# Optimization experiments

Hardware: AMD Instinct MI355X
Metric: run time of the kernel (lower is better)

The kernel has to match this reference:

```python
import jax, jax.numpy as jnp
import numpy as np

B, H, W, C = 8, 64, 64, 256  # NHWC, SAGAN-style feature map


def setup_inputs() -> dict:
    key = jax.random.key(0)
    ks = jax.random.split(key, 10)
    d_qk, d_v = C // 8, C // 2
    sc = lambda fan_in: 1.0 / np.sqrt(fan_in)
    return {
        "x": jax.random.normal(ks[0], (B, H, W, C), dtype=jnp.float32),
        "Wf": jax.random.normal(ks[1], (C, d_qk), dtype=jnp.float32) * sc(C),
        "bf": jnp.zeros((d_qk,), dtype=jnp.float32),
        "Wg": jax.random.normal(ks[2], (C, d_qk), dtype=jnp.float32) * sc(C),
        "bg": jnp.zeros((d_qk,), dtype=jnp.float32),
        "Wh": jax.random.normal(ks[3], (C, d_v), dtype=jnp.float32) * sc(C),
        "bh": jnp.zeros((d_v,), dtype=jnp.float32),
        "Wo": jax.random.normal(ks[4], (d_v, C), dtype=jnp.float32) * sc(d_v),
        "bo": jnp.zeros((C,), dtype=jnp.float32),
        # original inits gamma=0.0 (identity fwd); use nonzero so fwd exercises attention
        "gamma": jnp.float32(0.5),
    }


def reference(x, Wf, bf, Wg, bg, Wh, bh, Wo, bo, gamma):
    b, h_, w_, c = x.shape
    n = h_ * w_
    xf = x.reshape(b, n, c)  # 1x1 convs are per-pixel GEMMs
    f = xf @ Wf + bf          # [B, N, C/8]  (keys)
    g = xf @ Wg + bg          # [B, N, C/8]  (queries)
    hv = xf @ Wh + bh         # [B, N, C/2]  (values)
    s = jnp.einsum('bnd,bmd->bnm', g, f)   # unscaled scores [B, N, N]
    beta = jax.nn.softmax(s, axis=-1)
    o = jnp.einsum('bnm,bmd->bnd', beta, hv)  # [B, N, C/2]
    o = o @ Wo + bo                           # output 1x1 conv -> [B, N, C]
    out = gamma * o + xf
    return out.reshape(b, h_, w_, c)
```

## Files before the change

kernel.cpp:

```cpp
#include <hip/hip_runtime.h>
#include <hip/hip_bf16.h>

#define NB   8
#define CC   256
#define NN   4096
#define NTOT (NB*NN)
#define DQK  32
#define DV   128

typedef __attribute__((ext_vector_type(8))) short bf16x8;
typedef __attribute__((ext_vector_type(4))) float f32x4;
typedef __attribute__((ext_vector_type(16))) float f32x16;
typedef __attribute__((ext_vector_type(4))) float float4v;
typedef __attribute__((ext_vector_type(4))) unsigned int u32x4;

__device__ __forceinline__ short f2bf(float f) {
    __hip_bfloat16 h = __float2bfloat16(f);
    return *reinterpret_cast<short*>(&h);
}
__device__ __forceinline__ float bf2f(short s) {
    unsigned int u = ((unsigned int)(unsigned short)s) << 16;
    return __builtin_bit_cast(float, u);
}
__device__ __forceinline__ unsigned int cvtpk(float lo, float hi) {
    unsigned int r;
    asm("v_cvt_pk_bf16_f32 %0, %1, %2" : "=v"(r) : "v"(lo), "v"(hi));
    return r;
}
__device__ __forceinline__ void plswap(unsigned int &a, unsigned int &b) {
    asm("v_permlane32_swap_b32 %0, %1" : "+v"(a), "+v"(b));
}

#define OFF_F     0u
#define OFF_G     (2u<<20)
#define OFF_VT    (4u<<20)
#define OFF_OP    (12u<<20)
#define OFF_LS    (28u<<20)
#define OFF_WQKVT ((28u<<20)+(512u<<10))
#define OFF_WOT   (OFF_WQKVT + 192u*256u*2u)

__global__ __launch_bounds__(256) void prep_kernel(
    const float* __restrict__ Wf, const float* __restrict__ Wg,
    const float* __restrict__ Wh, const float* __restrict__ Wo,
    short* __restrict__ WqkvT, short* __restrict__ WoT)
{
    int idx = blockIdx.x * 256 + threadIdx.x;
    if (idx < 192 * 256) {
        int j = idx >> 8, k = idx & 255;
        float v = (j < 32) ? Wf[k * 32 + j]
                : (j < 64) ? Wg[k * 32 + (j - 32)]
                           : Wh[k * 128 + (j - 64)];
        WqkvT[j * 256 + k] = f2bf(v);
    }
    int i2 = idx - 192 * 256;
    if (i2 >= 0 && i2 < 256 * 128) {
        int c = i2 >> 7, d = i2 & 127;
        WoT[c * 128 + d] = f2bf(Wo[d * 256 + c]);
    }
}

__global__ __launch_bounds__(256) void proj_kernel(
    const float* __restrict__ x,
    const float* __restrict__ bf_, const float* __restrict__ bg_,
    const float* __restrict__ bh_,
    const short* __restrict__ WqkvT,
    short* __restrict__ fws, short* __restrict__ gws, short* __restrict__ vtile)
{
    int wid = threadIdx.x >> 6, lane = threadIdx.x & 63;
    int col16 = lane & 15, rq = lane >> 4;
    int rbase = blockIdx.x * 64 + wid * 16;
    int arow = rbase + col16;

    f32x4 acc[12];
    #pragma unroll
    for (int i = 0; i < 12; ++i) acc[i] = (f32x4){0.f, 0.f, 0.f, 0.f};

    const float* xrow = x + (size_t)arow * CC;
    #pragma unroll
    for (int kk = 0; kk < 8; ++kk) {
        int k0 = kk * 32 + rq * 8;
        float4v u0 = *(const float4v*)(xrow + k0);
        float4v u1 = *(const float4v*)(xrow + k0 + 4);
        bf16x8 av;
        av[0]=f2bf(u0[0]); av[1]=f2bf(u0[1]); av[2]=f2bf(u0[2]); av[3]=f2bf(u0[3]);
        av[4]=f2bf(u1[0]); av[5]=f2bf(u1[1]); av[6]=f2bf(u1[2]); av[7]=f2bf(u1[3]);
        #pragma unroll
        for (int nf = 0; nf < 12; ++nf) {
            bf16x8 bv = *(const bf16x8*)(WqkvT + (nf * 16 + col16) * 256 + k0);
            acc[nf] = __builtin_amdgcn_mfma_f32_16x16x32_bf16(av, bv, acc[nf], 0, 0, 0);
        }
    }

    #pragma unroll
    for (int nf = 0; nf < 12; ++nf) {
        int colg = nf * 16 + col16;
        #pragma unroll
        for (int r = 0; r < 4; ++r) {
            int rowg = rbase + rq * 4 + r;
            float val = acc[nf][r];
            if (colg < 32) {
                fws[(size_t)rowg * DQK + colg] = f2bf(val + bf_[colg]);
            } else if (colg < 64) {
                int c = colg - 32;
                gws[(size_t)rowg * DQK + c] = f2bf((val + bg_[c]) * 1.44269504089f);
            } else {
                int d = colg - 64;
                int b = rowg >> 12, n = rowg & 4095;
                int kt = n >> 6, kslot = (n >> 4) & 3, klh = (n >> 3) & 1, j = n & 7;
                size_t addr = (((size_t)(b * 64 + kt) * 4 + kslot) * 2048)
                            + (d >> 5) * 512 + klh * 256 + (d & 31) * 8 + j;
                vtile[addr] = f2bf(val + bh_[d]);
            }
        }
    }
}

__global__ __launch_bounds__(256, 4) void attn_kernel(
    const short* __restrict__ fws, const short* __restrict__ gws,
    const short* __restrict__ vtile, short* __restrict__ opart,
    float* __restrict__ lspart)
{
    __shared__ __align__(16) char smem[33280];

    int t = threadIdx.x;
    int wid = t >> 6, lane = t & 63;
    int l31 = lane & 31, lh = lane >> 5;
    int qh = wid >> 1, kh = wid & 1;

    int bid = blockIdx.x;
    int sid = (bid & 7) * 128 + (bid >> 3);
    int b = sid >> 7, rem = sid & 127;
    int ksh = rem >> 6, qt = rem & 63;
    int qbase = b * NN + qt * 64;
    int k0 = ksh * 32, kend = k0 + 32;

    const short* grow = gws + (size_t)(qbase + qh * 32 + l31) * DQK;
    bf16x8 gb0 = *(const bf16x8*)(grow + lh * 8);
    bf16x8 gb1 = *(const bf16x8*)(grow + 16 + lh * 8);

    int foff = (kh * 32 + l31) * DQK + lh * 8;
    const short* fS = fws + (size_t)b * NN * DQK;
    bf16x8 fc0 = *(const bf16x8*)(fS + (size_t)k0 * 2048 + foff);
    bf16x8 fc1 = *(const bf16x8*)(fS + (size_t)k0 * 2048 + foff + 16);

    f32x16 oaccT[4], zero16;
    #pragma unroll
    for (int i = 0; i < 16; ++i) {
        zero16[i] = 0.f;
        oaccT[0][i] = 0.f; oaccT[1][i] = 0.f; oaccT[2][i] = 0.f; oaccT[3][i] = 0.f;
    }
    float lsum = 0.f;

    for (int kb = k0; kb < kend; ++kb) {
        const short* fnp = fS + (size_t)(kb + 1) * 2048 + foff;
        bf16x8 fn0 = *(const bf16x8*)(fnp);
        bf16x8 fn1 = *(const bf16x8*)(fnp + 16);

        f32x16 s = __builtin_amdgcn_mfma_f32_32x32x16_bf16(fc0, gb0, zero16, 0, 0, 0);
        s = __builtin_amdgcn_mfma_f32_32x32x16_bf16(fc1, gb1, s, 0, 0, 0);

        unsigned int w[8];
        #pragma unroll
        for (int i = 0; i < 8; ++i) {
            float pa = __builtin_exp2f(s[2 * i]);
            float pb = __builtin_exp2f(s[2 * i + 1]);
            lsum += pa + pb;
            w[i] = cvtpk(pa, pb);
        }
        plswap(w[0], w[2]); plswap(w[1], w[3]);
        plswap(w[4], w[6]); plswap(w[5], w[7]);

        const short* vb_kb = vtile + (((size_t)(b * 64 + kb) * 4 + kh * 2) * 2048)
                           + (size_t)lane * 8;
        #pragma unroll
        for (int ks = 0; ks < 2; ++ks) {
            u32x4 pw = { w[ks * 4], w[ks * 4 + 1], w[ks * 4 + 2], w[ks * 4 + 3] };
            bf16x8 pb_ = __builtin_bit_cast(bf16x8, pw);
            #pragma unroll
            for (int dt = 0; dt < 4; ++dt) {
                bf16x8 va = *(const bf16x8*)(vb_kb + ks * 2048 + dt * 512);
                oaccT[dt] = __builtin_amdgcn_mfma_f32_32x32x16_bf16(va, pb_, oaccT[dt], 0, 0, 0);
            }
        }
        fc0 = fn0; fc1 = fn1;
    }

    lsum += __shfl_xor(lsum, 32);
    float* lsbuf = (float*)(&smem[32768]);
    if (lh == 0) lsbuf[(qh * 2 + kh) * 32 + l31] = lsum;
    __syncthreads();

    char* obuf = smem;
    if (kh == 1) {
        #pragma unroll
        for (int dt = 0; dt < 4; ++dt) {
            #pragma unroll
            for (int r = 0; r < 16; ++r) {
                int d = dt * 32 + (r & 3) + 8 * (r >> 2) + 4 * lh;
                int q = qh * 32 + l31;
                int byte = q * 512 + ((((d >> 2) ^ (q & 31)) << 4) | ((d & 3) << 2));
                *(float*)(obuf + byte) = oaccT[dt][r];
            }
        }
    }
    __syncthreads();
    if (kh == 0) {
        float tot = lsbuf[qh * 64 + l31] + lsbuf[qh * 64 + 32 + l31];
        if (lh == 0) lspart[(size_t)(qbase + qh * 32 + l31) * 2 + ksh] = tot;
        float iv = 1.f / tot;
        #pragma unroll
        for (int dt = 0; dt < 4; ++dt) {
            #pragma unroll
            for (int r = 0; r < 16; ++r) {
                int d = dt * 32 + (r & 3) + 8 * (r >> 2) + 4 * lh;
                int q = qh * 32 + l31;
                int byte = q * 512 + ((((d >> 2) ^ (q & 31)) << 4) | ((d & 3) << 2));
                float* p = (float*)(obuf + byte);
                *p = (*p + oaccT[dt][r]) * iv;
            }
        }
    }
    __syncthreads();
    {
        int q = t >> 2, dg = t & 3;
        size_t orow = ((size_t)(qbase + q) * 2 + ksh) * 128 + dg * 32;
        #pragma unroll
        for (int cc = 0; cc < 8; cc += 2) {
            int c0 = dg * 8 + cc;
            f32x4 u0 = *(const f32x4*)(obuf + q * 512 + (((c0 ^ (q & 31)) << 4)));
            f32x4 u1 = *(const f32x4*)(obuf + q * 512 + ((((c0 + 1) ^ (q & 31)) << 4)));
            bf16x8 ov;
            ov[0]=f2bf(u0[0]); ov[1]=f2bf(u0[1]); ov[2]=f2bf(u0[2]); ov[3]=f2bf(u0[3]);
            ov[4]=f2bf(u1[0]); ov[5]=f2bf(u1[1]); ov[6]=f2bf(u1[2]); ov[7]=f2bf(u1[3]);
            *(bf16x8*)(opart + orow + cc * 4) = ov;
        }
    }
}

__global__ __launch_bounds__(256) void out_kernel(
    const short* __restrict__ opart, const float* __restrict__ lspart,
    const short* __restrict__ WoT,
    const float* __restrict__ bo, const float* __restrict__ gamma,
    const float* __restrict__ x, float* __restrict__ out)
{
    int wid = threadIdx.x >> 6, lane = threadIdx.x & 63;
    int col16 = lane & 15, rq = lane >> 4;
    int rbase = blockIdx.x * 64 + wid * 16;
    int arow = rbase + col16;

    float l0 = lspart[(size_t)arow * 2];
    float l1 = lspart[(size_t)arow * 2 + 1];
    float iv = 1.f / (l0 + l1);
    float w0 = l0 * iv, w1 = l1 * iv;

    const short* oprow = opart + (size_t)arow * 256;
    bf16x8 afr[4];
    #pragma unroll
    for (int kk = 0; kk < 4; ++kk) {
        bf16x8 a0 = *(const bf16x8*)(oprow + kk * 32 + rq * 8);
        bf16x8 a1 = *(const bf16x8*)(oprow + 128 + kk * 32 + rq * 8);
        bf16x8 af;
        #pragma unroll
        for (int j = 0; j < 8; ++j)
            af[j] = f2bf(w0 * bf2f(a0[j]) + w1 * bf2f(a1[j]));
        afr[kk] = af;
    }

    f32x4 acc[16];
    #pragma unroll
    for (int i = 0; i < 16; ++i) acc[i] = (f32x4){0.f, 0.f, 0.f, 0.f};

    #pragma unroll
    for (int nf = 0; nf < 16; ++nf) {
        #pragma unroll
        for (int kk = 0; kk < 4; ++kk) {
            bf16x8 bfr = *(const bf16x8*)(WoT + (nf * 16 + col16) * DV + kk * 32 + rq * 8);
            acc[nf] = __builtin_amdgcn_mfma_f32_16x16x32_bf16(afr[kk], bfr, acc[nf], 0, 0, 0);
        }
    }

    float gm = gamma[0];
    #pragma unroll
    for (int nf = 0; nf < 16; ++nf) {
        int colg = nf * 16 + col16;
        float bov = bo[colg];
        #pragma unroll
        for (int r = 0; r < 4; ++r) {
            int rowg = rbase + rq * 4 + r;
            out[(size_t)rowg * CC + colg] = gm * (acc[nf][r] + bov) + x[(size_t)rowg * CC + colg];
        }
    }
}

extern "C" void kernel_launch(void* const* d_in, const int* in_sizes, int n_in,
                              void* d_out, int out_size, void* d_ws, size_t ws_size,
                              hipStream_t stream)
{
    const float* x     = (const float*)d_in[0];
    const float* Wf    = (const float*)d_in[1];
    const float* bf_   = (const float*)d_in[2];
    const float* Wg    = (const float*)d_in[3];
    const float* bg_   = (const float*)d_in[4];
    const float* Wh    = (const float*)d_in[5];
    const float* bh_   = (const float*)d_in[6];
    const float* Wo    = (const float*)d_in[7];
    const float* bo    = (const float*)d_in[8];
    const float* gamma = (const float*)d_in[9];

    char* ws = (char*)d_ws;
    short* fws   = (short*)(ws + OFF_F);
    short* gws   = (short*)(ws + OFF_G);
    short* vtile = (short*)(ws + OFF_VT);
    short* opart = (short*)(ws + OFF_OP);
    float* lsp   = (float*)(ws + OFF_LS);
    short* WqkvT = (short*)(ws + OFF_WQKVT);
    short* WoT   = (short*)(ws + OFF_WOT);
    float* out   = (float*)d_out;

    hipLaunchKernelGGL(prep_kernel, dim3(320), dim3(256), 0, stream, Wf, Wg, Wh, Wo, WqkvT, WoT);
    hipLaunchKernelGGL(proj_kernel, dim3(512), dim3(256), 0, stream,
                       x, bf_, bg_, bh_, WqkvT, fws, gws, vtile);
    hipLaunchKernelGGL(attn_kernel, dim3(1024), dim3(256), 0, stream, fws, gws, vtile, opart, lsp);
    hipLaunchKernelGGL(out_kernel, dim3(512), dim3(256), 0, stream, opart, lsp, WoT, bo, gamma, x, out);
}
```

Baseline: 139.3 us.

## Double-buffer F and V register loads in attention loop with MFMA priority boost

The attention inner loop now prefetches both the key (F) fragments and all eight V fragments for the next key block into a second register set, alternating two buffers so global loads overlap the current block's MFMAs and exp work. Before, V was loaded just ahead of use. The PV MFMAs are wrapped in s_setprio to favour matrix issue, and launch bounds drop from 4 to 3 waves per SIMD to make room for the extra registers. The cost is lower occupancy and more VGPR pressure; loads at the loop tail are clamped to the last block, which adds a few redundant loads.

```diff
diff --git a/kernel.cpp b/kernel.cpp
--- a/kernel.cpp
+++ b/kernel.cpp
@@ -115,7 +115,7 @@
     }
 }
 
-__global__ __launch_bounds__(256, 4) void attn_kernel(
+__global__ __launch_bounds__(256, 3) void attn_kernel(
     const short* __restrict__ fws, const short* __restrict__ gws,
     const short* __restrict__ vtile, short* __restrict__ opart,
     float* __restrict__ lspart)
@@ -140,8 +140,8 @@
 
     int foff = (kh * 32 + l31) * DQK + lh * 8;
     const short* fS = fws + (size_t)b * NN * DQK;
-    bf16x8 fc0 = *(const bf16x8*)(fS + (size_t)k0 * 2048 + foff);
-    bf16x8 fc1 = *(const bf16x8*)(fS + (size_t)k0 * 2048 + foff + 16);
+    const short* vS = vtile + ((size_t)b * 64 * 4) * 2048 + (kh * 2) * 2048
+                    + (size_t)lane * 8;
 
     f32x16 oaccT[4], zero16;
     #pragma unroll
@@ -151,39 +151,63 @@
     }
     float lsum = 0.f;
 
-    for (int kb = k0; kb < kend; ++kb) {
-        const short* fnp = fS + (size_t)(kb + 1) * 2048 + foff;
-        bf16x8 fn0 = *(const bf16x8*)(fnp);
-        bf16x8 fn1 = *(const bf16x8*)(fnp + 16);
-
-        f32x16 s = __builtin_amdgcn_mfma_f32_32x32x16_bf16(fc0, gb0, zero16, 0, 0, 0);
-        s = __builtin_amdgcn_mfma_f32_32x32x16_bf16(fc1, gb1, s, 0, 0, 0);
-
-        unsigned int w[8];
-        #pragma unroll
-        for (int i = 0; i < 8; ++i) {
-            float pa = __builtin_exp2f(s[2 * i]);
-            float pb = __builtin_exp2f(s[2 * i + 1]);
-            lsum += pa + pb;
-            w[i] = cvtpk(pa, pb);
-        }
-        plswap(w[0], w[2]); plswap(w[1], w[3]);
-        plswap(w[4], w[6]); plswap(w[5], w[7]);
-
-        const short* vb_kb = vtile + (((size_t)(b * 64 + kb) * 4 + kh * 2) * 2048)
-                           + (size_t)lane * 8;
-        #pragma unroll
-        for (int ks = 0; ks < 2; ++ks) {
-            u32x4 pw = { w[ks * 4], w[ks * 4 + 1], w[ks * 4 + 2], w[ks * 4 + 3] };
-            bf16x8 pb_ = __builtin_bit_cast(bf16x8, pw);
-            #pragma unroll
-            for (int dt = 0; dt < 4; ++dt) {
-                bf16x8 va = *(const bf16x8*)(vb_kb + ks * 2048 + dt * 512);
-                oaccT[dt] = __builtin_amdgcn_mfma_f32_32x32x16_bf16(va, pb_, oaccT[dt], 0, 0, 0);
-            }
-        }
-        fc0 = fn0; fc1 = fn1;
-    }
+#define LOADSET(F0, F1, V0, V1, V2, V3, V4, V5, V6, V7, KB) {              \
+    int kc_ = (KB) < kend ? (KB) : kend - 1;                               \
+    const short* fp_ = fS + (size_t)kc_ * 2048 + foff;                     \
+    F0 = *(const bf16x8*)(fp_);                                            \
+    F1 = *(const bf16x8*)(fp_ + 16);                                       \
+    const short* vp_ = vS + (size_t)kc_ * 8192;                            \
+    V0 = *(const bf16x8*)(vp_);                                            \
+    V1 = *(const bf16x8*)(vp_ + 512);                                      \
+    V2 = *(const bf16x8*)(vp_ + 1024);                                     \
+    V3 = *(const bf16x8*)(vp_ + 1536);                                     \
+    V4 = *(const bf16x8*)(vp_ + 2048);                                     \
+    V5 = *(const bf16x8*)(vp_ + 2560);                                     \
+    V6 = *(const bf16x8*)(vp_ + 3072);                                     \
+    V7 = *(const bf16x8*)(vp_ + 3584);                                     \
+}
+
+#define COMPUTE(F0, F1, V0, V1, V2, V3, V4, V5, V6, V7) {                  \
+    f32x16 s_ = __builtin_amdgcn_mfma_f32_32x32x16_bf16(F0, gb0, zero16, 0, 0, 0); \
+    s_ = __builtin_amdgcn_mfma_f32_32x32x16_bf16(F1, gb1, s_, 0, 0, 0);    \
+    unsigned int w_[8];                                                    \
+    _Pragma("unroll")                                                      \
+    for (int i_ = 0; i_ < 8; ++i_) {                                       \
+        float pa_ = __builtin_exp2f(s_[2 * i_]);                           \
+        float pb_ = __builtin_exp2f(s_[2 * i_ + 1]);                       \
+        lsum += pa_ + pb_;                                                 \
+        w_[i_] = cvtpk(pa_, pb_);                                          \
+    }                                                                      \
+    plswap(w_[0], w_[2]); plswap(w_[1], w_[3]);                            \
+    plswap(w_[4], w_[6]); plswap(w_[5], w_[7]);                            \
+    u32x4 pw0_ = { w_[0], w_[1], w_[2], w_[3] };                           \
+    u32x4 pw1_ = { w_[4], w_[5], w_[6], w_[7] };                           \
+    bf16x8 p0_ = __builtin_bit_cast(bf16x8, pw0_);                         \
+    bf16x8 p1_ = __builtin_bit_cast(bf16x8, pw1_);                         \
+    __builtin_amdgcn_s_setprio(1);                                         \
+    oaccT[0] = __builtin_amdgcn_mfma_f32_32x32x16_bf16(V0, p0_, oaccT[0], 0, 0, 0); \
+    oaccT[1] = __builtin_amdgcn_mfma_f32_32x32x16_bf16(V1, p0_, oaccT[1], 0, 0, 0); \
+    oaccT[2] = __builtin_amdgcn_mfma_f32_32x32x16_bf16(V2, p0_, oaccT[2], 0, 0, 0); \
+    oaccT[3] = __builtin_amdgcn_mfma_f32_32x32x16_bf16(V3, p0_, oaccT[3], 0, 0, 0); \
+    oaccT[0] = __builtin_amdgcn_mfma_f32_32x32x16_bf16(V4, p1_, oaccT[0], 0, 0, 0); \
+    oaccT[1] = __builtin_amdgcn_mfma_f32_32x32x16_bf16(V5, p1_, oaccT[1], 0, 0, 0); \
+    oaccT[2] = __builtin_amdgcn_mfma_f32_32x32x16_bf16(V6, p1_, oaccT[2], 0, 0, 0); \
+    oaccT[3] = __builtin_amdgcn_mfma_f32_32x32x16_bf16(V7, p1_, oaccT[3], 0, 0, 0); \
+    __builtin_amdgcn_s_setprio(0);                                         \
+}
+
+    bf16x8 fa0, fa1, a0, a1, a2, a3, a4, a5, a6, a7;
+    bf16x8 fb0, fb1, b0, b1, b2, b3, b4, b5, b6, b7;
+
+    LOADSET(fa0, fa1, a0, a1, a2, a3, a4, a5, a6, a7, k0);
+    for (int kb = k0; kb < kend; kb += 2) {
+        LOADSET(fb0, fb1, b0, b1, b2, b3, b4, b5, b6, b7, kb + 1);
+        COMPUTE(fa0, fa1, a0, a1, a2, a3, a4, a5, a6, a7);
+        LOADSET(fa0, fa1, a0, a1, a2, a3, a4, a5, a6, a7, kb + 2);
+        COMPUTE(fb0, fb1, b0, b1, b2, b3, b4, b5, b6, b7);
+    }
+#undef LOADSET
+#undef COMPUTE
 
     lsum += __shfl_xor(lsum, 32);
     float* lsbuf = (float*)(&smem[32768]);
```

Result: slower. 256.5 us (+84.1%).

## Fuse output projection into attention kernel and split keys across waves

Applied to the files above, without the earlier changes.

Merges the attention and output-projection kernels. Each block now handles 32 queries over all 4096 keys, with the four waves striding over key tiles and reducing their partial accumulators through shared memory. The normalized result is written to LDS as bf16 and multiplied by Wo with MFMA, followed by the bias, gamma and residual epilogue. This removes the opart/lspart round trip through global memory and one launch, and adds setprio hints around the PV MFMAs. In exchange it adds an in-block cross-wave reduction, and each block now reads the whole key/value set for only 32 queries.

```diff
diff --git a/kernel.cpp b/kernel.cpp
--- a/kernel.cpp
+++ b/kernel.cpp
@@ -13,14 +13,11 @@
 typedef __attribute__((ext_vector_type(16))) float f32x16;
 typedef __attribute__((ext_vector_type(4))) float float4v;
 typedef __attribute__((ext_vector_type(4))) unsigned int u32x4;
+typedef __attribute__((ext_vector_type(2))) unsigned int u32x2;
 
 __device__ __forceinline__ short f2bf(float f) {
     __hip_bfloat16 h = __float2bfloat16(f);
     return *reinterpret_cast<short*>(&h);
-}
-__device__ __forceinline__ float bf2f(short s) {
-    unsigned int u = ((unsigned int)(unsigned short)s) << 16;
-    return __builtin_bit_cast(float, u);
 }
 __device__ __forceinline__ unsigned int cvtpk(float lo, float hi) {
     unsigned int r;
@@ -34,9 +31,7 @@
 #define OFF_F     0u
 #define OFF_G     (2u<<20)
 #define OFF_VT    (4u<<20)
-#define OFF_OP    (12u<<20)
-#define OFF_LS    (28u<<20)
-#define OFF_WQKVT ((28u<<20)+(512u<<10))
+#define OFF_WQKVT (12u<<20)
 #define OFF_WOT   (OFF_WQKVT + 192u*256u*2u)
 
 __global__ __launch_bounds__(256) void prep_kernel(
@@ -115,33 +110,29 @@
     }
 }
 
-__global__ __launch_bounds__(256, 4) void attn_kernel(
+__global__ __launch_bounds__(256, 4) void attn_fused_kernel(
     const short* __restrict__ fws, const short* __restrict__ gws,
-    const short* __restrict__ vtile, short* __restrict__ opart,
-    float* __restrict__ lspart)
+    const short* __restrict__ vtile, const short* __restrict__ WoT,
+    const float* __restrict__ bo, const float* __restrict__ gamma,
+    const float* __restrict__ x, float* __restrict__ out)
 {
     __shared__ __align__(16) char smem[33280];
 
     int t = threadIdx.x;
     int wid = t >> 6, lane = t & 63;
     int l31 = lane & 31, lh = lane >> 5;
-    int qh = wid >> 1, kh = wid & 1;
 
     int bid = blockIdx.x;
     int sid = (bid & 7) * 128 + (bid >> 3);
-    int b = sid >> 7, rem = sid & 127;
-    int ksh = rem >> 6, qt = rem & 63;
-    int qbase = b * NN + qt * 64;
-    int k0 = ksh * 32, kend = k0 + 32;
-
-    const short* grow = gws + (size_t)(qbase + qh * 32 + l31) * DQK;
+    int b = sid >> 7, qt = sid & 127;
+    int nbase = qt * 32;
+
+    const short* grow = gws + (size_t)(b * NN + nbase + l31) * DQK;
     bf16x8 gb0 = *(const bf16x8*)(grow + lh * 8);
     bf16x8 gb1 = *(const bf16x8*)(grow + 16 + lh * 8);
 
-    int foff = (kh * 32 + l31) * DQK + lh * 8;
-    const short* fS = fws + (size_t)b * NN * DQK;
-    bf16x8 fc0 = *(const bf16x8*)(fS + (size_t)k0 * 2048 + foff);
-    bf16x8 fc1 = *(const bf16x8*)(fS + (size_t)k0 * 2048 + foff + 16);
+    const short* fS = fws + (size_t)b * NN * DQK + l31 * DQK + lh * 8;
+    const short* vS = vtile + (size_t)b * 524288 + (size_t)lane * 8;
 
     f32x16 oaccT[4], zero16;
     #pragma unroll
@@ -151,145 +142,135 @@
     }
     float lsum = 0.f;
 
-    for (int kb = k0; kb < kend; ++kb) {
-        const short* fnp = fS + (size_t)(kb + 1) * 2048 + foff;
-        bf16x8 fn0 = *(const bf16x8*)(fnp);
-        bf16x8 fn1 = *(const bf16x8*)(fnp + 16);
-
-        f32x16 s = __builtin_amdgcn_mfma_f32_32x32x16_bf16(fc0, gb0, zero16, 0, 0, 0);
-        s = __builtin_amdgcn_mfma_f32_32x32x16_bf16(fc1, gb1, s, 0, 0, 0);
-
-        unsigned int w[8];
-        #pragma unroll
-        for (int i = 0; i < 8; ++i) {
-            float pa = __builtin_exp2f(s[2 * i]);
-            float pb = __builtin_exp2f(s[2 * i + 1]);
-            lsum += pa + pb;
-            w[i] = cvtpk(pa, pb);
-        }
-        plswap(w[0], w[2]); plswap(w[1], w[3]);
-        plswap(w[4], w[6]); plswap(w[5], w[7]);
-
-        const short* vb_kb = vtile + (((size_t)(b * 64 + kb) * 4 + kh * 2) * 2048)
-                           + (size_t)lane * 8;
-        #pragma unroll
-        for (int ks = 0; ks < 2; ++ks) {
-            u32x4 pw = { w[ks * 4], w[ks * 4 + 1], w[ks * 4 + 2], w[ks * 4 + 3] };
-            bf16x8 pb_ = __builtin_bit_cast(bf16x8, pw);
-            #pragma unroll
-            for (int dt = 0; dt < 4; ++dt) {
-                bf16x8 va = *(const bf16x8*)(vb_kb + ks * 2048 + dt * 512);
-                oaccT[dt] = __builtin_amdgcn_mfma_f32_32x32x16_bf16(va, pb_, oaccT[dt], 0, 0, 0);
-            }
-        }
+#define HALF_BODY(FC0, FC1, KT, H) {                                            \
+    f32x16 s_ = __builtin_amdgcn_mfma_f32_32x32x16_bf16(FC0, gb0, zero16, 0, 0, 0); \
+    s_ = __builtin_amdgcn_mfma_f32_32x32x16_bf16(FC1, gb1, s_, 0, 0, 0);        \
+    unsigned int w_[8];                                                         \
+    _Pragma("unroll")                                                           \
+    for (int i_ = 0; i_ < 8; ++i_) {                                            \
+        float pa_ = __builtin_exp2f(s_[2 * i_]);                                \
+        float pb_ = __builtin_exp2f(s_[2 * i_ + 1]);                            \
+        lsum += pa_ + pb_;                                                      \
+        w_[i_] = cvtpk(pa_, pb_);                                               \
+    }                                                                           \
+    plswap(w_[0], w_[2]); plswap(w_[1], w_[3]);                                 \
+    plswap(w_[4], w_[6]); plswap(w_[5], w_[7]);                                 \
+    u32x4 pw0_ = { w_[0], w_[1], w_[2], w_[3] };                                \
+    u32x4 pw1_ = { w_[4], w_[5], w_[6], w_[7] };                                \
+    bf16x8 p0_ = __builtin_bit_cast(bf16x8, pw0_);                              \
+    bf16x8 p1_ = __builtin_bit_cast(bf16x8, pw1_);                              \
+    const short* vp_ = vS + (size_t)(KT) * 8192 + (H) * 4096;                   \
+    __builtin_amdgcn_s_setprio(1);                                              \
+    oaccT[0] = __builtin_amdgcn_mfma_f32_32x32x16_bf16(*(const bf16x8*)(vp_),        p0_, oaccT[0], 0, 0, 0); \
+    oaccT[1] = __builtin_amdgcn_mfma_f32_32x32x16_bf16(*(const bf16x8*)(vp_ + 512),  p0_, oaccT[1], 0, 0, 0); \
+    oaccT[2] = __builtin_amdgcn_mfma_f32_32x32x16_bf16(*(const bf16x8*)(vp_ + 1024), p0_, oaccT[2], 0, 0, 0); \
+    oaccT[3] = __builtin_amdgcn_mfma_f32_32x32x16_bf16(*(const bf16x8*)(vp_ + 1536), p0_, oaccT[3], 0, 0, 0); \
+    oaccT[0] = __builtin_amdgcn_mfma_f32_32x32x16_bf16(*(const bf16x8*)(vp_ + 2048), p1_, oaccT[0], 0, 0, 0); \
+    oaccT[1] = __builtin_amdgcn_mfma_f32_32x32x16_bf16(*(const bf16x8*)(vp_ + 2560), p1_, oaccT[1], 0, 0, 0); \
+    oaccT[2] = __builtin_amdgcn_mfma_f32_32x32x16_bf16(*(const bf16x8*)(vp_ + 3072), p1_, oaccT[2], 0, 0, 0); \
+    oaccT[3] = __builtin_amdgcn_mfma_f32_32x32x16_bf16(*(const bf16x8*)(vp_ + 3584), p1_, oaccT[3], 0, 0, 0); \
+    __builtin_amdgcn_s_setprio(0);                                              \
+}
+
+    bf16x8 fc0 = *(const bf16x8*)(fS + (size_t)wid * 2048);
+    bf16x8 fc1 = *(const bf16x8*)(fS + (size_t)wid * 2048 + 16);
+
+    for (int kt = wid; kt < 64; kt += 4) {
+        const short* fp1 = fS + (size_t)kt * 2048 + 1024;
+        bf16x8 fn0 = *(const bf16x8*)(fp1);
+        bf16x8 fn1 = *(const bf16x8*)(fp1 + 16);
+        HALF_BODY(fc0, fc1, kt, 0);
         fc0 = fn0; fc1 = fn1;
-    }
+        int ktn = (kt + 4 < 64) ? kt + 4 : kt;
+        const short* fp0 = fS + (size_t)ktn * 2048;
+        fn0 = *(const bf16x8*)(fp0);
+        fn1 = *(const bf16x8*)(fp0 + 16);
+        HALF_BODY(fc0, fc1, kt, 1);
+        fc0 = fn0; fc1 = fn1;
+    }
+#undef HALF_BODY
 
     lsum += __shfl_xor(lsum, 32);
-    float* lsbuf = (float*)(&smem[32768]);
-    if (lh == 0) lsbuf[(qh * 2 + kh) * 32 + l31] = lsum;
+    float* lsbuf = (float*)(smem + 32768);
+    if (lh == 0) lsbuf[wid * 32 + l31] = lsum;
+
+    char* regA = smem;
+    char* regB = smem + 16384;
+
+#define DUMP(BASE) {                                                            \
+    _Pragma("unroll")                                                           \
+    for (int dt_ = 0; dt_ < 4; ++dt_) {                                         \
+        _Pragma("unroll")                                                       \
+        for (int g_ = 0; g_ < 4; ++g_) {                                        \
+            f32x4 ch_ = { oaccT[dt_][4*g_], oaccT[dt_][4*g_+1],                 \
+                          oaccT[dt_][4*g_+2], oaccT[dt_][4*g_+3] };             \
+            int c_ = dt_ * 4 + g_;                                              \
+            *(f32x4*)((BASE) + lane * 256 + ((c_ ^ ((lane & 7) << 1)) << 4)) = ch_; \
+        }                                                                       \
+    }                                                                           \
+}
+#define ADDIN(BASE) {                                                           \
+    _Pragma("unroll")                                                           \
+    for (int dt_ = 0; dt_ < 4; ++dt_) {                                         \
+        _Pragma("unroll")                                                       \
+        for (int g_ = 0; g_ < 4; ++g_) {                                        \
+            int c_ = dt_ * 4 + g_;                                              \
+            f32x4 ch_ = *(const f32x4*)((BASE) + lane * 256 + ((c_ ^ ((lane & 7) << 1)) << 4)); \
+            oaccT[dt_][4*g_]   += ch_[0]; oaccT[dt_][4*g_+1] += ch_[1];         \
+            oaccT[dt_][4*g_+2] += ch_[2]; oaccT[dt_][4*g_+3] += ch_[3];         \
+        }                                                                       \
+    }                                                                           \
+}
+
+    if (wid == 2) DUMP(regA);
+    if (wid == 3) DUMP(regB);
     __syncthreads();
-
-    char* obuf = smem;
-    if (kh == 1) {
+    if (wid == 0) ADDIN(regA);
+    if (wid == 1) ADDIN(regB);
+    __syncthreads();
+    if (wid == 1) DUMP(regA);
+    __syncthreads();
+    if (wid == 0) {
+        ADDIN(regA);
+        float tot = lsbuf[l31] + lsbuf[32 + l31] + lsbuf[64 + l31] + lsbuf[96 + l31];
+        float iv = 1.0f / tot;
         #pragma unroll
         for (int dt = 0; dt < 4; ++dt) {
             #pragma unroll
-            for (int r = 0; r < 16; ++r) {
-                int d = dt * 32 + (r & 3) + 8 * (r >> 2) + 4 * lh;
-                int q = qh * 32 + l31;
-                int byte = q * 512 + ((((d >> 2) ^ (q & 31)) << 4) | ((d & 3) << 2));
-                *(float*)(obuf + byte) = oaccT[dt][r];
+            for (int g = 0; g < 4; ++g) {
+                float v0 = oaccT[dt][4*g]   * iv, v1 = oaccT[dt][4*g+1] * iv;
+                float v2 = oaccT[dt][4*g+2] * iv, v3 = oaccT[dt][4*g+3] * iv;
+                u32x2 wv = { cvtpk(v0, v1), cvtpk(v2, v3) };
+                int c = dt * 4 + g;
+                *(u32x2*)(regB + l31 * 256 + ((c ^ (l31 & 15)) << 4) + lh * 8) = wv;
             }
         }
     }
     __syncthreads();
-    if (kh == 0) {
-        float tot = lsbuf[qh * 64 + l31] + lsbuf[qh * 64 + 32 + l31];
-        if (lh == 0) lspart[(size_t)(qbase + qh * 32 + l31) * 2 + ksh] = tot;
-        float iv = 1.f / tot;
-        #pragma unroll
-        for (int dt = 0; dt < 4; ++dt) {
-            #pragma unroll
-            for (int r = 0; r < 16; ++r) {
-                int d = dt * 32 + (r & 3) + 8 * (r >> 2) + 4 * lh;
-                int q = qh * 32 + l31;
-                int byte = q * 512 + ((((d >> 2) ^ (q & 31)) << 4) | ((d & 3) << 2));
-                float* p = (float*)(obuf + byte);
-                *p = (*p + oaccT[dt][r]) * iv;
-            }
-        }
-    }
-    __syncthreads();
-    {
-        int q = t >> 2, dg = t & 3;
-        size_t orow = ((size_t)(qbase + q) * 2 + ksh) * 128 + dg * 32;
-        #pragma unroll
-        for (int cc = 0; cc < 8; cc += 2) {
-            int c0 = dg * 8 + cc;
-            f32x4 u0 = *(const f32x4*)(obuf + q * 512 + (((c0 ^ (q & 31)) << 4)));
-            f32x4 u1 = *(const f32x4*)(obuf + q * 512 + ((((c0 + 1) ^ (q & 31)) << 4)));
-            bf16x8 ov;
-            ov[0]=f2bf(u0[0]); ov[1]=f2bf(u0[1]); ov[2]=f2bf(u0[2]); ov[3]=f2bf(u0[3]);
-            ov[4]=f2bf(u1[0]); ov[5]=f2bf(u1[1]); ov[6]=f2bf(u1[2]); ov[7]=f2bf(u1[3]);
-            *(bf16x8*)(opart + orow + cc * 4) = ov;
-        }
-    }
-}
-
-__global__ __launch_bounds__(256) void out_kernel(
-    const short* __restrict__ opart, const float* __restrict__ lspart,
-    const short* __restrict__ WoT,
-    const float* __restrict__ bo, const float* __restrict__ gamma,
-    const float* __restrict__ x, float* __restrict__ out)
-{
-    int wid = threadIdx.x >> 6, lane = threadIdx.x & 63;
-    int col16 = lane & 15, rq = lane >> 4;
-    int rbase = blockIdx.x * 64 + wid * 16;
-    int arow = rbase + col16;
-
-    float l0 = lspart[(size_t)arow * 2];
-    float l1 = lspart[(size_t)arow * 2 + 1];
-    float iv = 1.f / (l0 + l1);
-    float w0 = l0 * iv, w1 = l1 * iv;
-
-    const short* oprow = opart + (size_t)arow * 256;
-    bf16x8 afr[4];
-    #pragma unroll
-    for (int kk = 0; kk < 4; ++kk) {
-        bf16x8 a0 = *(const bf16x8*)(oprow + kk * 32 + rq * 8);
-        bf16x8 a1 = *(const bf16x8*)(oprow + 128 + kk * 32 + rq * 8);
-        bf16x8 af;
-        #pragma unroll
-        for (int j = 0; j < 8; ++j)
-            af[j] = f2bf(w0 * bf2f(a0[j]) + w1 * bf2f(a1[j]));
-        afr[kk] = af;
-    }
-
-    f32x4 acc[16];
-    #pragma unroll
-    for (int i = 0; i < 16; ++i) acc[i] = (f32x4){0.f, 0.f, 0.f, 0.f};
-
-    #pragma unroll
-    for (int nf = 0; nf < 16; ++nf) {
-        #pragma unroll
-        for (int kk = 0; kk < 4; ++kk) {
-            bf16x8 bfr = *(const bf16x8*)(WoT + (nf * 16 + col16) * DV + kk * 32 + rq * 8);
-            acc[nf] = __builtin_amdgcn_mfma_f32_16x16x32_bf16(afr[kk], bfr, acc[nf], 0, 0, 0);
-        }
-    }
 
     float gm = gamma[0];
     #pragma unroll
-    for (int nf = 0; nf < 16; ++nf) {
-        int colg = nf * 16 + col16;
-        float bov = bo[colg];
-        #pragma unroll
-        for (int r = 0; r < 4; ++r) {
-            int rowg = rbase + rq * 4 + r;
-            out[(size_t)rowg * CC + colg] = gm * (acc[nf][r] + bov) + x[(size_t)rowg * CC + colg];
-        }
-    }
+    for (int ni = 0; ni < 2; ++ni) {
+        int nt = wid * 2 + ni;
+        f32x16 acc = zero16;
+        #pragma unroll
+        for (int cs = 0; cs < 8; ++cs) {
+            bf16x8 af = *(const bf16x8*)(regB + l31 * 256 +
+                                         (((cs * 2 + lh) ^ (l31 & 15)) << 4));
+            bf16x8 bf_ = *(const bf16x8*)(WoT + (nt * 32 + l31) * 128 + cs * 16 + lh * 8);
+            acc = __builtin_amdgcn_mfma_f32_32x32x16_bf16(af, bf_, acc, 0, 0, 0);
+        }
+        int col = nt * 32 + l31;
+        float bov = bo[col];
+        #pragma unroll
+        for (int r = 0; r < 16; ++r) {
+            int q = (r & 3) + 8 * (r >> 2) + 4 * lh;
+            size_t rowg = (size_t)(b * NN + nbase + q);
+            out[rowg * CC + col] = gm * (acc[r] + bov) + x[rowg * CC + col];
+        }
+    }
+#undef DUMP
+#undef ADDIN
 }
 
 extern "C" void kernel_launch(void* const* d_in, const int* in_sizes, int n_in,
@@ -311,8 +292,6 @@
     short* fws   = (short*)(ws + OFF_F);
     short* gws   = (short*)(ws + OFF_G);
     short* vtile = (short*)(ws + OFF_VT);
-    short* opart = (short*)(ws + OFF_OP);
-    float* lsp   = (float*)(ws + OFF_LS);
     short* WqkvT = (short*)(ws + OFF_WQKVT);
     short* WoT   = (short*)(ws + OFF_WOT);
     float* out   = (float*)d_out;
@@ -320,6 +299,6 @@
     hipLaunchKernelGGL(prep_kernel, dim3(320), dim3(256), 0, stream, Wf, Wg, Wh, Wo, WqkvT, WoT);
     hipLaunchKernelGGL(proj_kernel, dim3(512), dim3(256), 0, stream,
                        x, bf_, bg_, bh_, WqkvT, fws, gws, vtile);
-    hipLaunchKernelGGL(attn_kernel, dim3(1024), dim3(256), 0, stream, fws, gws, vtile, opart, lsp);
-    hipLaunchKernelGGL(out_kernel, dim3(512), dim3(256), 0, stream, opart, lsp, WoT, bo, gamma, x, out);
-}
+    hipLaunchKernelGGL(attn_fused_kernel, dim3(1024), dim3(256), 0, stream,
+                       fws, gws, vtile, WoT, bo, gamma, x, out);
+}
```

Result: slower. 179.1 us (+28.5%).

## Vectorize projection and output epilogues via swapped MFMA operands and LDS transpose

Applied to the files above, without the earlier changes.

Swaps the MFMA A/B operands in the projection and output GEMMs so each lane holds four consecutive output columns of one row. The epilogues can then write 4-wide vectors instead of scattered scalar stores. The value tensor is staged through shared memory and written to its tiled layout as 16-byte stores. The attention kernel's V addressing is simplified to a per-batch base pointer with constant offsets. The intent is to cut uncoalesced global store and load traffic, at the cost of an LDS buffer and a barrier in the projection kernel.

```diff
diff --git a/kernel.cpp b/kernel.cpp
--- a/kernel.cpp
+++ b/kernel.cpp
@@ -9,6 +9,7 @@
 #define DV   128
 
 typedef __attribute__((ext_vector_type(8))) short bf16x8;
+typedef __attribute__((ext_vector_type(4))) short s16x4;
 typedef __attribute__((ext_vector_type(4))) float f32x4;
 typedef __attribute__((ext_vector_type(16))) float f32x16;
 typedef __attribute__((ext_vector_type(4))) float float4v;
@@ -66,10 +67,13 @@
     const short* __restrict__ WqkvT,
     short* __restrict__ fws, short* __restrict__ gws, short* __restrict__ vtile)
 {
+    __shared__ short hlds[128 * 72];
+
     int wid = threadIdx.x >> 6, lane = threadIdx.x & 63;
     int col16 = lane & 15, rq = lane >> 4;
-    int rbase = blockIdx.x * 64 + wid * 16;
-    int arow = rbase + col16;
+    int nloc = wid * 16 + col16;
+    int arow = blockIdx.x * 64 + nloc;
+    int b = blockIdx.x >> 6, kt = blockIdx.x & 63;
 
     f32x4 acc[12];
     #pragma unroll
@@ -87,31 +91,48 @@
         #pragma unroll
         for (int nf = 0; nf < 12; ++nf) {
             bf16x8 bv = *(const bf16x8*)(WqkvT + (nf * 16 + col16) * 256 + k0);
-            acc[nf] = __builtin_amdgcn_mfma_f32_16x16x32_bf16(av, bv, acc[nf], 0, 0, 0);
-        }
-    }
-
-    #pragma unroll
-    for (int nf = 0; nf < 12; ++nf) {
-        int colg = nf * 16 + col16;
-        #pragma unroll
-        for (int r = 0; r < 4; ++r) {
-            int rowg = rbase + rq * 4 + r;
-            float val = acc[nf][r];
-            if (colg < 32) {
-                fws[(size_t)rowg * DQK + colg] = f2bf(val + bf_[colg]);
-            } else if (colg < 64) {
-                int c = colg - 32;
-                gws[(size_t)rowg * DQK + c] = f2bf((val + bg_[c]) * 1.44269504089f);
-            } else {
-                int d = colg - 64;
-                int b = rowg >> 12, n = rowg & 4095;
-                int kt = n >> 6, kslot = (n >> 4) & 3, klh = (n >> 3) & 1, j = n & 7;
-                size_t addr = (((size_t)(b * 64 + kt) * 4 + kslot) * 2048)
-                            + (d >> 5) * 512 + klh * 256 + (d & 31) * 8 + j;
-                vtile[addr] = f2bf(val + bh_[d]);
-            }
-        }
+            acc[nf] = __builtin_amdgcn_mfma_f32_16x16x32_bf16(bv, av, acc[nf], 0, 0, 0);
+        }
+    }
+
+    #pragma unroll
+    for (int nf = 0; nf < 2; ++nf) {
+        int c0 = nf * 16 + rq * 4;
+        float4v b4 = *(const float4v*)(bf_ + c0);
+        s16x4 v = { f2bf(acc[nf][0] + b4[0]), f2bf(acc[nf][1] + b4[1]),
+                    f2bf(acc[nf][2] + b4[2]), f2bf(acc[nf][3] + b4[3]) };
+        *(s16x4*)(fws + (size_t)arow * DQK + c0) = v;
+    }
+    #pragma unroll
+    for (int nf = 2; nf < 4; ++nf) {
+        int c0 = (nf - 2) * 16 + rq * 4;
+        float4v b4 = *(const float4v*)(bg_ + c0);
+        s16x4 v = { f2bf((acc[nf][0] + b4[0]) * 1.44269504089f),
+                    f2bf((acc[nf][1] + b4[1]) * 1.44269504089f),
+                    f2bf((acc[nf][2] + b4[2]) * 1.44269504089f),
+                    f2bf((acc[nf][3] + b4[3]) * 1.44269504089f) };
+        *(s16x4*)(gws + (size_t)arow * DQK + c0) = v;
+    }
+
+    #pragma unroll
+    for (int nf = 4; nf < 12; ++nf) {
+        int d0 = (nf - 4) * 16 + rq * 4;
+        float4v b4 = *(const float4v*)(bh_ + d0);
+        #pragma unroll
+        for (int r = 0; r < 4; ++r)
+            hlds[(d0 + r) * 72 + nloc] = f2bf(acc[nf][r] + b4[r]);
+    }
+    __syncthreads();
+
+    int t = threadIdx.x;
+    int l31 = t & 31, dt = (t >> 5) & 3, klh = t >> 7;
+    int d = dt * 32 + l31;
+    #pragma unroll
+    for (int kslot = 0; kslot < 4; ++kslot) {
+        bf16x8 v = *(const bf16x8*)(&hlds[d * 72 + kslot * 16 + klh * 8]);
+        size_t addr = (((size_t)(b * 64 + kt) * 4 + kslot) * 2048)
+                    + dt * 512 + klh * 256 + l31 * 8;
+        *(bf16x8*)(vtile + addr) = v;
     }
 }
 
@@ -140,8 +161,8 @@
 
     int foff = (kh * 32 + l31) * DQK + lh * 8;
     const short* fS = fws + (size_t)b * NN * DQK;
-    bf16x8 fc0 = *(const bf16x8*)(fS + (size_t)k0 * 2048 + foff);
-    bf16x8 fc1 = *(const bf16x8*)(fS + (size_t)k0 * 2048 + foff + 16);
+    const short* vS = vtile + ((size_t)b * 64 * 4) * 2048 + (kh * 2) * 2048
+                    + (size_t)lane * 8;
 
     f32x16 oaccT[4], zero16;
     #pragma unroll
@@ -150,6 +171,9 @@
         oaccT[0][i] = 0.f; oaccT[1][i] = 0.f; oaccT[2][i] = 0.f; oaccT[3][i] = 0.f;
     }
     float lsum = 0.f;
+
+    bf16x8 fc0 = *(const bf16x8*)(fS + (size_t)k0 * 2048 + foff);
+    bf16x8 fc1 = *(const bf16x8*)(fS + (size_t)k0 * 2048 + foff + 16);
 
     for (int kb = k0; kb < kend; ++kb) {
         const short* fnp = fS + (size_t)(kb + 1) * 2048 + foff;
@@ -170,18 +194,21 @@
         plswap(w[0], w[2]); plswap(w[1], w[3]);
         plswap(w[4], w[6]); plswap(w[5], w[7]);
 
-        const short* vb_kb = vtile + (((size_t)(b * 64 + kb) * 4 + kh * 2) * 2048)
-                           + (size_t)lane * 8;
-        #pragma unroll
-        for (int ks = 0; ks < 2; ++ks) {
-            u32x4 pw = { w[ks * 4], w[ks * 4 + 1], w[ks * 4 + 2], w[ks * 4 + 3] };
-            bf16x8 pb_ = __builtin_bit_cast(bf16x8, pw);
-            #pragma unroll
-            for (int dt = 0; dt < 4; ++dt) {
-                bf16x8 va = *(const bf16x8*)(vb_kb + ks * 2048 + dt * 512);
-                oaccT[dt] = __builtin_amdgcn_mfma_f32_32x32x16_bf16(va, pb_, oaccT[dt], 0, 0, 0);
-            }
-        }
+        u32x4 pw0 = { w[0], w[1], w[2], w[3] };
+        u32x4 pw1 = { w[4], w[5], w[6], w[7] };
+        bf16x8 p0 = __builtin_bit_cast(bf16x8, pw0);
+        bf16x8 p1 = __builtin_bit_cast(bf16x8, pw1);
+
+        const short* vp = vS + (size_t)kb * 8192;
+        oaccT[0] = __builtin_amdgcn_mfma_f32_32x32x16_bf16(*(const bf16x8*)(vp),        p0, oaccT[0], 0, 0, 0);
+        oaccT[1] = __builtin_amdgcn_mfma_f32_32x32x16_bf16(*(const bf16x8*)(vp + 512),  p0, oaccT[1], 0, 0, 0);
+        oaccT[2] = __builtin_amdgcn_mfma_f32_32x32x16_bf16(*(const bf16x8*)(vp + 1024), p0, oaccT[2], 0, 0, 0);
+        oaccT[3] = __builtin_amdgcn_mfma_f32_32x32x16_bf16(*(const bf16x8*)(vp + 1536), p0, oaccT[3], 0, 0, 0);
+        oaccT[0] = __builtin_amdgcn_mfma_f32_32x32x16_bf16(*(const bf16x8*)(vp + 2048), p1, oaccT[0], 0, 0, 0);
+        oaccT[1] = __builtin_amdgcn_mfma_f32_32x32x16_bf16(*(const bf16x8*)(vp + 2560), p1, oaccT[1], 0, 0, 0);
+        oaccT[2] = __builtin_amdgcn_mfma_f32_32x32x16_bf16(*(const bf16x8*)(vp + 3072), p1, oaccT[2], 0, 0, 0);
+        oaccT[3] = __builtin_amdgcn_mfma_f32_32x32x16_bf16(*(const bf16x8*)(vp + 3584), p1, oaccT[3], 0, 0, 0);
+
         fc0 = fn0; fc1 = fn1;
     }
 
@@ -245,8 +272,7 @@
 {
     int wid = threadIdx.x >> 6, lane = threadIdx.x & 63;
     int col16 = lane & 15, rq = lane >> 4;
-    int rbase = blockIdx.x * 64 + wid * 16;
-    int arow = rbase + col16;
+    int arow = blockIdx.x * 64 + wid * 16 + col16;
 
     float l0 = lspart[(size_t)arow * 2];
     float l1 = lspart[(size_t)arow * 2 + 1];
@@ -254,7 +280,7 @@
     float w0 = l0 * iv, w1 = l1 * iv;
 
     const short* oprow = opart + (size_t)arow * 256;
-    bf16x8 afr[4];
+    bf16x8 bfr[4];
     #pragma unroll
     for (int kk = 0; kk < 4; ++kk) {
         bf16x8 a0 = *(const bf16x8*)(oprow + kk * 32 + rq * 8);
@@ -263,7 +289,7 @@
         #pragma unroll
         for (int j = 0; j < 8; ++j)
             af[j] = f2bf(w0 * bf2f(a0[j]) + w1 * bf2f(a1[j]));
-        afr[kk] = af;
+        bfr[kk] = af;
     }
 
     f32x4 acc[16];
@@ -274,21 +300,24 @@
     for (int nf = 0; nf < 16; ++nf) {
         #pragma unroll
         for (int kk = 0; kk < 4; ++kk) {
-            bf16x8 bfr = *(const bf16x8*)(WoT + (nf * 16 + col16) * DV + kk * 32 + rq * 8);
-            acc[nf] = __builtin_amdgcn_mfma_f32_16x16x32_bf16(afr[kk], bfr, acc[nf], 0, 0, 0);
+            bf16x8 wfr = *(const bf16x8*)(WoT + (nf * 16 + col16) * DV + kk * 32 + rq * 8);
+            acc[nf] = __builtin_amdgcn_mfma_f32_16x16x32_bf16(wfr, bfr[kk], acc[nf], 0, 0, 0);
         }
     }
 
     float gm = gamma[0];
+    const float* xrow = x + (size_t)arow * CC;
+    float* orow_ = out + (size_t)arow * CC;
     #pragma unroll
     for (int nf = 0; nf < 16; ++nf) {
-        int colg = nf * 16 + col16;
-        float bov = bo[colg];
-        #pragma unroll
-        for (int r = 0; r < 4; ++r) {
-            int rowg = rbase + rq * 4 + r;
-            out[(size_t)rowg * CC + colg] = gm * (acc[nf][r] + bov) + x[(size_t)rowg * CC + colg];
-        }
+        int c0 = nf * 16 + rq * 4;
+        float4v bo4 = *(const float4v*)(bo + c0);
+        float4v xv = *(const float4v*)(xrow + c0);
+        float4v ov;
+        #pragma unroll
+        for (int r = 0; r < 4; ++r)
+            ov[r] = gm * (acc[nf][r] + bo4[r]) + xv[r];
+        *(float4v*)(orow_ + c0) = ov;
     }
 }
 
```

New measurement: 173.0 us. 24.2% more time.
